# Kernel optimization log

Hardware: AMD Instinct MI355X
Metric: run time of the kernel (lower is better)

Reference implementation:

```python
import jax, jax.numpy as jnp
import numpy as np

DIM = 1024
H = 16
HD = 64

def setup_inputs() -> dict:
    key = jax.random.key(0)
    ks = jax.random.split(key, 5)
    x = jax.random.normal(ks[0], (2, 2048, DIM), dtype=jnp.float32)
    gamma = jnp.ones((DIM,), jnp.float32)
    beta = jnp.zeros((DIM,), jnp.float32)
    w_qkv = jax.random.normal(ks[1], (DIM, 3 * H * HD), dtype=jnp.float32) * (DIM ** -0.5)
    w_out = jax.random.normal(ks[2], (H * HD, DIM), dtype=jnp.float32) * ((H * HD) ** -0.5)
    b_out = jnp.zeros((DIM,), jnp.float32)
    return {"x": x, "gamma": gamma, "beta": beta, "w_qkv": w_qkv, "w_out": w_out, "b_out": b_out}

def reference(x, gamma, beta, w_qkv, w_out, b_out):
    # LayerNorm (pre-norm)
    mu = jnp.mean(x, axis=-1, keepdims=True)
    var = jnp.var(x, axis=-1, keepdims=True)
    xn = (x - mu) * jax.lax.rsqrt(var + 1e-5) * gamma + beta
    # QKV projection (no bias)
    qkv = xn @ w_qkv  # (b, n, 3*h*hd)
    q, k, v = jnp.split(qkv, 3, axis=-1)
    b, n, _ = x.shape
    split = lambda t: t.reshape(b, n, H, HD).transpose(0, 2, 1, 3)  # b h n d
    q, k, v = split(q), split(k), split(v)
    scale = HD ** -0.5
    scores = jnp.einsum('bhqd,bhkd->bhqk', q, k) * scale
    weights = jax.nn.softmax(scores, axis=-1)
    attn = jnp.einsum('bhqk,bhkd->bhqd', weights, v)  # b h n d
    attn = attn.transpose(0, 2, 1, 3).reshape(b, n, H * HD)
    # output projection (dropout is identity in eval)
    return attn @ w_out + b_out
```

## Files before the change

### kernel.cpp

```cpp
#include <hip/hip_runtime.h>
#include <hip/hip_bf16.h>


typedef _Float16 f16x8 __attribute__((ext_vector_type(8)));
typedef _Float16 f16x4 __attribute__((ext_vector_type(4)));
typedef float    f32x4 __attribute__((ext_vector_type(4)));

#define DIM   1024
#define NH    16
#define HD2   64
#define SEQ   2048
#define ROWS  4096
#define QKVN  3072

__device__ __forceinline__ void async_copy16(void* lds, const void* gsrc) {
    __builtin_amdgcn_global_load_lds(
        (const __attribute__((address_space(1))) unsigned int*)gsrc,
        (__attribute__((address_space(3))) unsigned int*)lds, 16, 0, 0);
}

__global__ __launch_bounds__(256) void prologue_kernel(
    const float* __restrict__ x, const float* __restrict__ gamma,
    const float* __restrict__ beta, _Float16* __restrict__ xn,
    const float* __restrict__ w_qkv, _Float16* __restrict__ wqkvT,
    const float* __restrict__ w_out, _Float16* __restrict__ woutT) {
    __shared__ float smem[32 * 33];
    const int bid = blockIdx.x;
    const int t = threadIdx.x;
    if (bid < ROWS) {
        const int row = bid;
        const float4 v = reinterpret_cast<const float4*>(x + (size_t)row * DIM)[t];
        float s1 = v.x + v.y + v.z + v.w;
        float s2 = v.x * v.x + v.y * v.y + v.z * v.z + v.w * v.w;
        for (int off = 32; off; off >>= 1) {
            s1 += __shfl_down(s1, off);
            s2 += __shfl_down(s2, off);
        }
        const int wv = t >> 6, lane = t & 63;
        if (lane == 0) { smem[wv * 2] = s1; smem[wv * 2 + 1] = s2; }
        __syncthreads();
        s1 = smem[0] + smem[2] + smem[4] + smem[6];
        s2 = smem[1] + smem[3] + smem[5] + smem[7];
        const float mu = s1 * (1.0f / DIM);
        const float var = s2 * (1.0f / DIM) - mu * mu;
        const float rstd = rsqrtf(var + 1e-5f);
        const float4 g = reinterpret_cast<const float4*>(gamma)[t];
        const float4 bb = reinterpret_cast<const float4*>(beta)[t];
        f16x4 o;
        o[0] = (_Float16)((v.x - mu) * rstd * g.x + bb.x);
        o[1] = (_Float16)((v.y - mu) * rstd * g.y + bb.y);
        o[2] = (_Float16)((v.z - mu) * rstd * g.z + bb.z);
        o[3] = (_Float16)((v.w - mu) * rstd * g.w + bb.w);
        reinterpret_cast<f16x4*>(xn + (size_t)row * DIM)[t] = o;
        return;
    }
    const float* in;
    _Float16* out;
    int C, bx, by;
    if (bid < ROWS + (QKVN / 32) * (DIM / 32)) {
        const int q = bid - ROWS;
        in = w_qkv; out = wqkvT; C = QKVN;
        bx = q % (QKVN / 32); by = q / (QKVN / 32);
    } else {
        const int q = bid - ROWS - (QKVN / 32) * (DIM / 32);
        in = w_out; out = woutT; C = DIM;
        bx = q % (DIM / 32); by = q / (DIM / 32);
    }
    const int R = DIM;
    const int c0 = bx * 32, r0 = by * 32;
    const int tx = t & 31, ty = t >> 5;
    float (*tile)[33] = reinterpret_cast<float(*)[33]>(smem);
#pragma unroll
    for (int i = 0; i < 4; i++)
        tile[ty + i * 8][tx] = in[(size_t)(r0 + ty + i * 8) * C + c0 + tx];
    __syncthreads();
#pragma unroll
    for (int i = 0; i < 4; i++)
        out[(size_t)(c0 + ty + i * 8) * R + r0 + tx] = (_Float16)tile[tx][ty + i * 8];
}

__global__ __launch_bounds__(256) void gemm_qkv_kernel(
    const _Float16* __restrict__ A, const _Float16* __restrict__ Bt,
    _Float16* __restrict__ qk, _Float16* __restrict__ vT, int K) {
    __shared__ _Float16 Al[2][128 * 32];
    __shared__ _Float16 Bl[2][128 * 32];
    const int t = threadIdx.x, wv = t >> 6, lane = t & 63;
    const int lg = lane >> 4, lr = lane & 15;
    const int wr = wv >> 1, wc = wv & 1;
    const int m0 = blockIdx.y * 128, n0 = blockIdx.x * 128;

    f32x4 acc[4][4] = {};

    const int srow = t >> 2, sk = (t & 3) * 8;
    const _Float16* Ag0 = A + (size_t)(m0 + srow) * K + sk;
    const _Float16* Bg0 = Bt + (size_t)(n0 + srow) * K + sk;

    auto STAGE = [&](int buf, int k0) {
        _Float16* Alw = &Al[buf][wv * 512];
        _Float16* Blw = &Bl[buf][wv * 512];
        async_copy16(Alw,        Ag0 + k0);
        async_copy16(Alw + 2048, Ag0 + (size_t)64 * K + k0);
        async_copy16(Blw,        Bg0 + k0);
        async_copy16(Blw + 2048, Bg0 + (size_t)64 * K + k0);
    };

    STAGE(0, 0);
    asm volatile("s_waitcnt vmcnt(0)" ::: "memory");
    __builtin_amdgcn_s_barrier();
    int cur = 0;
    for (int k0 = 0; k0 < K; k0 += 32) {
        if (k0 + 32 < K) STAGE(cur ^ 1, k0 + 32);
        const _Float16* Ab = &Al[cur][0];
        const _Float16* Bb = &Bl[cur][0];
        f16x8 af[4], bfr[4];
#pragma unroll
        for (int m = 0; m < 4; m++)
            af[m] = *reinterpret_cast<const f16x8*>(&Ab[(wr * 64 + m * 16 + lr) * 32 + lg * 8]);
#pragma unroll
        for (int n = 0; n < 4; n++)
            bfr[n] = *reinterpret_cast<const f16x8*>(&Bb[(wc * 64 + n * 16 + lr) * 32 + lg * 8]);
#pragma unroll
        for (int m = 0; m < 4; m++)
#pragma unroll
            for (int n = 0; n < 4; n++)
                acc[m][n] = __builtin_amdgcn_mfma_f32_16x16x32_f16(af[m], bfr[n], acc[m][n], 0, 0, 0);
        asm volatile("s_waitcnt vmcnt(0)" ::: "memory");
        __builtin_amdgcn_s_barrier();
        cur ^= 1;
    }

    if (n0 < 2 * DIM) {
#pragma unroll
        for (int m = 0; m < 4; m++) {
            const int row = m0 + wr * 64 + m * 16 + lg * 4;
#pragma unroll
            for (int n = 0; n < 4; n++) {
                const int col = n0 + wc * 64 + n * 16 + lr;
#pragma unroll
                for (int jj = 0; jj < 4; jj++)
                    qk[(size_t)(row + jj) * 2048 + col] = (_Float16)acc[m][n][jj];
            }
        }
    } else {
#pragma unroll
        for (int m = 0; m < 4; m++) {
            const int row = m0 + wr * 64 + m * 16 + lg * 4;
            const int b = row >> 11, nn = row & 2047;
#pragma unroll
            for (int n = 0; n < 4; n++) {
                const int vcol = n0 + wc * 64 + n * 16 + lr - 2 * DIM;
                f16x4 pk;
#pragma unroll
                for (int jj = 0; jj < 4; jj++) pk[jj] = (_Float16)acc[m][n][jj];
                *reinterpret_cast<f16x4*>(&vT[(size_t)(b * 1024 + vcol) * SEQ + nn]) = pk;
            }
        }
    }
}

__global__ __launch_bounds__(256) void gemm_out_kernel(
    const _Float16* __restrict__ A, const _Float16* __restrict__ Bt,
    float* __restrict__ C, const float* __restrict__ bias, int N, int K) {
    __shared__ _Float16 Al[2][128 * 32];
    __shared__ _Float16 Bl[2][64 * 32];
    const int t = threadIdx.x, wv = t >> 6, lane = t & 63;
    const int lg = lane >> 4, lr = lane & 15;
    const int wr = wv >> 1, wc = wv & 1;
    const int m0 = blockIdx.y * 128, n0 = blockIdx.x * 64;

    f32x4 acc[4][2] = {};

    const int srow = t >> 2, sk = (t & 3) * 8;
    const _Float16* Ag0 = A + (size_t)(m0 + srow) * K + sk;
    const _Float16* Bg0 = Bt + (size_t)(n0 + srow) * K + sk;

    auto STAGE = [&](int buf, int k0) {
        _Float16* Alw = &Al[buf][wv * 512];
        _Float16* Blw = &Bl[buf][wv * 512];
        async_copy16(Alw,        Ag0 + k0);
        async_copy16(Alw + 2048, Ag0 + (size_t)64 * K + k0);
        async_copy16(Blw,        Bg0 + k0);
    };

    STAGE(0, 0);
    asm volatile("s_waitcnt vmcnt(0)" ::: "memory");
    __builtin_amdgcn_s_barrier();
    int cur = 0;
    for (int k0 = 0; k0 < K; k0 += 32) {
        if (k0 + 32 < K) STAGE(cur ^ 1, k0 + 32);
        const _Float16* Ab = &Al[cur][0];
        const _Float16* Bb = &Bl[cur][0];
        f16x8 af[4], bfr[2];
#pragma unroll
        for (int m = 0; m < 4; m++)
            af[m] = *reinterpret_cast<const f16x8*>(&Ab[(wr * 64 + m * 16 + lr) * 32 + lg * 8]);
#pragma unroll
        for (int n = 0; n < 2; n++)
            bfr[n] = *reinterpret_cast<const f16x8*>(&Bb[(wc * 32 + n * 16 + lr) * 32 + lg * 8]);
#pragma unroll
        for (int m = 0; m < 4; m++)
#pragma unroll
            for (int n = 0; n < 2; n++)
                acc[m][n] = __builtin_amdgcn_mfma_f32_16x16x32_f16(af[m], bfr[n], acc[m][n], 0, 0, 0);
        asm volatile("s_waitcnt vmcnt(0)" ::: "memory");
        __builtin_amdgcn_s_barrier();
        cur ^= 1;
    }

#pragma unroll
    for (int m = 0; m < 4; m++) {
        const int row = m0 + wr * 64 + m * 16 + lg * 4;
#pragma unroll
        for (int n = 0; n < 2; n++) {
            const int col = n0 + wc * 32 + n * 16 + lr;
            const float bo = bias[col];
#pragma unroll
            for (int jj = 0; jj < 4; jj++)
                C[(size_t)(row + jj) * N + col] = acc[m][n][jj] + bo;
        }
    }
}

__global__ __launch_bounds__(256, 2) void attn_fa_kernel(
    const _Float16* __restrict__ qk, const _Float16* __restrict__ vT,
    _Float16* __restrict__ attn) {
    const int id = blockIdx.x;
    const int nid = (id & 7) * 64 + (id >> 3);
    const int bh = nid >> 4, b = bh >> 4, h = bh & 15;
    const int q0 = (nid & 15) * 128;
    const int t = threadIdx.x, wv = t >> 6, lane = t & 63;
    const int lg = lane >> 4, lr = lane & 15;

    __shared__ _Float16 Kl[2][64][72];
    __shared__ _Float16 Vt[2][64][72];

    const _Float16* qb = qk + (size_t)(b * SEQ + q0 + wv * 32 + lr) * 2048 + h * HD2;
    f16x8 qf[2][2];
    qf[0][0] = *reinterpret_cast<const f16x8*>(qb + lg * 8);
    qf[0][1] = *reinterpret_cast<const f16x8*>(qb + 32 + lg * 8);
    qf[1][0] = *reinterpret_cast<const f16x8*>(qb + (size_t)16 * 2048 + lg * 8);
    qf[1][1] = *reinterpret_cast<const f16x8*>(qb + (size_t)16 * 2048 + 32 + lg * 8);
#pragma unroll
    for (int qs = 0; qs < 2; qs++) {
        qf[qs][0] = qf[qs][0] * (_Float16)0.125f;
        qf[qs][1] = qf[qs][1] * (_Float16)0.125f;
    }

    f32x4 o[2][4] = {};
    float mrun[2] = {-INFINITY, -INFINITY}, lrun[2] = {0.f, 0.f};

    const int sr = t >> 3, sc = (t & 7) * 8;
    const _Float16* kbase = qk + (size_t)(b * SEQ + sr) * 2048 + DIM + h * HD2 + sc;
    const _Float16* vbase = vT + (size_t)(bh * HD2 + sr) * SEQ + sc;

    f16x8 rk0 = *reinterpret_cast<const f16x8*>(kbase);
    f16x8 rk1 = *reinterpret_cast<const f16x8*>(kbase + (size_t)32 * 2048);
    f16x8 rv0 = *reinterpret_cast<const f16x8*>(vbase);
    f16x8 rv1 = *reinterpret_cast<const f16x8*>(vbase + (size_t)32 * SEQ);
    *reinterpret_cast<f16x8*>(&Kl[0][sr][sc])      = rk0;
    *reinterpret_cast<f16x8*>(&Kl[0][sr + 32][sc]) = rk1;
    *reinterpret_cast<f16x8*>(&Vt[0][sr][sc])      = rv0;
    *reinterpret_cast<f16x8*>(&Vt[0][sr + 32][sc]) = rv1;
    rk0 = *reinterpret_cast<const f16x8*>(kbase + (size_t)64 * 2048);
    rk1 = *reinterpret_cast<const f16x8*>(kbase + (size_t)96 * 2048);
    rv0 = *reinterpret_cast<const f16x8*>(vbase + 64);
    rv1 = *reinterpret_cast<const f16x8*>(vbase + (size_t)32 * SEQ + 64);
    asm volatile("s_waitcnt lgkmcnt(0)" ::: "memory");
    __builtin_amdgcn_s_barrier();

    int p = 0;
    for (int kv0 = 0; kv0 < SEQ; kv0 += 64, p ^= 1) {
        if (kv0 + 64 < SEQ) {
            *reinterpret_cast<f16x8*>(&Kl[p ^ 1][sr][sc])      = rk0;
            *reinterpret_cast<f16x8*>(&Kl[p ^ 1][sr + 32][sc]) = rk1;
            *reinterpret_cast<f16x8*>(&Vt[p ^ 1][sr][sc])      = rv0;
            *reinterpret_cast<f16x8*>(&Vt[p ^ 1][sr + 32][sc]) = rv1;
            if (kv0 + 128 < SEQ) {
                const _Float16* kp = kbase + (size_t)(kv0 + 128) * 2048;
                const _Float16* vp = vbase + (kv0 + 128);
                rk0 = *reinterpret_cast<const f16x8*>(kp);
                rk1 = *reinterpret_cast<const f16x8*>(kp + (size_t)32 * 2048);
                rv0 = *reinterpret_cast<const f16x8*>(vp);
                rv1 = *reinterpret_cast<const f16x8*>(vp + (size_t)32 * SEQ);
            }
        }

        f32x4 s[2][4];
#pragma unroll
        for (int n = 0; n < 4; n++) {
            f16x8 kf0 = *reinterpret_cast<const f16x8*>(&Kl[p][n * 16 + lr][lg * 8]);
            f16x8 kf1 = *reinterpret_cast<const f16x8*>(&Kl[p][n * 16 + lr][32 + lg * 8]);
            __builtin_amdgcn_s_setprio(1);
#pragma unroll
            for (int qs = 0; qs < 2; qs++) {
                f32x4 z = {0.f, 0.f, 0.f, 0.f};
                z = __builtin_amdgcn_mfma_f32_16x16x32_f16(kf0, qf[qs][0], z, 0, 0, 0);
                z = __builtin_amdgcn_mfma_f32_16x16x32_f16(kf1, qf[qs][1], z, 0, 0, 0);
                s[qs][n] = z;
            }
            __builtin_amdgcn_s_setprio(0);
        }

        f16x8 pa[2][2];
#pragma unroll
        for (int qs = 0; qs < 2; qs++) {
            float m1 = fmaxf(fmaxf(s[qs][0][0], s[qs][0][1]), fmaxf(s[qs][0][2], s[qs][0][3]));
#pragma unroll
            for (int n = 1; n < 4; n++)
                m1 = fmaxf(m1, fmaxf(fmaxf(s[qs][n][0], s[qs][n][1]), fmaxf(s[qs][n][2], s[qs][n][3])));
            m1 = fmaxf(m1, __shfl_xor(m1, 16));
            m1 = fmaxf(m1, __shfl_xor(m1, 32));
            if (!__all(m1 - mrun[qs] <= 8.f)) {
                const float mnew = fmaxf(mrun[qs], m1);
                const float corr = __expf(mrun[qs] - mnew);
                mrun[qs] = mnew;
                lrun[qs] *= corr;
#pragma unroll
                for (int dn = 0; dn < 4; dn++) o[qs][dn] *= corr;
            }
            float rsum = 0.f;
#pragma unroll
            for (int n = 0; n < 4; n++)
#pragma unroll
                for (int jj = 0; jj < 4; jj++) {
                    const float pv = __expf(s[qs][n][jj] - mrun[qs]);
                    s[qs][n][jj] = pv;
                    rsum += pv;
                }
            rsum += __shfl_xor(rsum, 16);
            rsum += __shfl_xor(rsum, 32);
            lrun[qs] += rsum;
#pragma unroll
            for (int m = 0; m < 2; m++) {
                f16x8 pv;
#pragma unroll
                for (int jj = 0; jj < 4; jj++) {
                    pv[jj]     = (_Float16)s[qs][2 * m][jj];
                    pv[4 + jj] = (_Float16)s[qs][2 * m + 1][jj];
                }
                pa[qs][m] = pv;
            }
        }

#pragma unroll
        for (int dn = 0; dn < 4; dn++) {
            const _Float16* vr = &Vt[p][dn * 16 + lr][0];
            f16x4 va0 = *reinterpret_cast<const f16x4*>(vr + lg * 4);
            f16x4 va1 = *reinterpret_cast<const f16x4*>(vr + 16 + lg * 4);
            f16x4 vb0 = *reinterpret_cast<const f16x4*>(vr + 32 + lg * 4);
            f16x4 vb1 = *reinterpret_cast<const f16x4*>(vr + 48 + lg * 4);
            f16x8 vf0, vf1;
#pragma unroll
            for (int j = 0; j < 4; j++) {
                vf0[j] = va0[j]; vf0[4 + j] = va1[j];
                vf1[j] = vb0[j]; vf1[4 + j] = vb1[j];
            }
            __builtin_amdgcn_s_setprio(1);
#pragma unroll
            for (int qs = 0; qs < 2; qs++) {
                o[qs][dn] = __builtin_amdgcn_mfma_f32_16x16x32_f16(vf0, pa[qs][0], o[qs][dn], 0, 0, 0);
                o[qs][dn] = __builtin_amdgcn_mfma_f32_16x16x32_f16(vf1, pa[qs][1], o[qs][dn], 0, 0, 0);
            }
            __builtin_amdgcn_s_setprio(0);
        }
        asm volatile("s_waitcnt lgkmcnt(0)" ::: "memory");
        __builtin_amdgcn_s_barrier();
    }

#pragma unroll
    for (int qs = 0; qs < 2; qs++) {
        const float inv = 1.0f / lrun[qs];
        const size_t orow = (size_t)(b * SEQ + q0 + wv * 32 + qs * 16 + lr);
#pragma unroll
        for (int dn = 0; dn < 4; dn++) {
            f16x4 pk;
#pragma unroll
            for (int jj = 0; jj < 4; jj++) pk[jj] = (_Float16)(o[qs][dn][jj] * inv);
            *reinterpret_cast<f16x4*>(&attn[orow * DIM + h * HD2 + dn * 16 + lg * 4]) = pk;
        }
    }
}

extern "C" void kernel_launch(void* const* d_in, const int* in_sizes, int n_in,
                              void* d_out, int out_size, void* d_ws, size_t ws_size,
                              hipStream_t stream) {
    const float* x     = (const float*)d_in[0];
    const float* gamma = (const float*)d_in[1];
    const float* beta  = (const float*)d_in[2];
    const float* w_qkv = (const float*)d_in[3];
    const float* w_out = (const float*)d_in[4];
    const float* b_out = (const float*)d_in[5];
    float* out = (float*)d_out;

    _Float16* ws    = (_Float16*)d_ws;
    _Float16* xn    = ws;
    _Float16* wqkvT = xn + (size_t)ROWS * DIM;
    _Float16* woutT = wqkvT + (size_t)QKVN * DIM;
    _Float16* qk    = woutT + (size_t)DIM * DIM;
    _Float16* vT    = qk + (size_t)ROWS * 2048;
    _Float16* attnb = xn;

    const int pro_blocks = ROWS + (QKVN / 32) * (DIM / 32) + (DIM / 32) * (DIM / 32);
    prologue_kernel<<<pro_blocks, 256, 0, stream>>>(x, gamma, beta, xn, w_qkv, wqkvT, w_out, woutT);
    gemm_qkv_kernel<<<dim3(QKVN / 128, ROWS / 128), 256, 0, stream>>>(xn, wqkvT, qk, vT, DIM);
    attn_fa_kernel<<<512, 256, 0, stream>>>(qk, vT, attnb);
    gemm_out_kernel<<<dim3(DIM / 64, ROWS / 128), 256, 0, stream>>>(attnb, woutT, out, b_out, DIM, DIM);
}
```

Before: 205.4 us.

## Halve attention query tile per block and remap GEMM blocks for XCD locality

The attention kernel now processes 64 query rows per block (16 per wave) instead of 128, doubling the grid to 1024 blocks and raising the occupancy hint to 4 blocks per CU. The LDS row pitch is padded from 72 to 76. Both GEMM kernels switch to a 1D grid with a swizzled block index so that consecutive blocks on each XCD share operand tiles. The aim is better CU utilization and L2 locality, at the cost of reloading each K/V tile twice as often per query.

New measurement: 208.9 us. About the same (+1.7%).

```diff
diff --git a/kernel.cpp b/kernel.cpp
--- a/kernel.cpp
+++ b/kernel.cpp
@@ -87,7 +87,10 @@
     const int t = threadIdx.x, wv = t >> 6, lane = t & 63;
     const int lg = lane >> 4, lr = lane & 15;
     const int wr = wv >> 1, wc = wv & 1;
-    const int m0 = blockIdx.y * 128, n0 = blockIdx.x * 128;
+    const int id = blockIdx.x;
+    const int nid = (id & 7) * 96 + (id >> 3);
+    const int bx = nid / 32, by = nid % 32;
+    const int m0 = by * 128, n0 = bx * 128;
 
     f32x4 acc[4][4] = {};
 
@@ -166,7 +169,10 @@
     const int t = threadIdx.x, wv = t >> 6, lane = t & 63;
     const int lg = lane >> 4, lr = lane & 15;
     const int wr = wv >> 1, wc = wv & 1;
-    const int m0 = blockIdx.y * 128, n0 = blockIdx.x * 64;
+    const int id = blockIdx.x;
+    const int nid = (id & 7) * 64 + (id >> 3);
+    const int bx = nid / 32, by = nid % 32;
+    const int m0 = by * 128, n0 = bx * 64;
 
     f32x4 acc[4][2] = {};
 
@@ -221,33 +227,27 @@
     }
 }
 
-__global__ __launch_bounds__(256, 2) void attn_fa_kernel(
+__global__ __launch_bounds__(256, 4) void attn_fa_kernel(
     const _Float16* __restrict__ qk, const _Float16* __restrict__ vT,
     _Float16* __restrict__ attn) {
     const int id = blockIdx.x;
-    const int nid = (id & 7) * 64 + (id >> 3);
-    const int bh = nid >> 4, b = bh >> 4, h = bh & 15;
-    const int q0 = (nid & 15) * 128;
+    const int nid = (id & 7) * 128 + (id >> 3);
+    const int bh = nid >> 5, b = bh >> 4, h = bh & 15;
+    const int q0 = (nid & 31) * 64;
     const int t = threadIdx.x, wv = t >> 6, lane = t & 63;
     const int lg = lane >> 4, lr = lane & 15;
 
-    __shared__ _Float16 Kl[2][64][72];
-    __shared__ _Float16 Vt[2][64][72];
-
-    const _Float16* qb = qk + (size_t)(b * SEQ + q0 + wv * 32 + lr) * 2048 + h * HD2;
-    f16x8 qf[2][2];
-    qf[0][0] = *reinterpret_cast<const f16x8*>(qb + lg * 8);
-    qf[0][1] = *reinterpret_cast<const f16x8*>(qb + 32 + lg * 8);
-    qf[1][0] = *reinterpret_cast<const f16x8*>(qb + (size_t)16 * 2048 + lg * 8);
-    qf[1][1] = *reinterpret_cast<const f16x8*>(qb + (size_t)16 * 2048 + 32 + lg * 8);
-#pragma unroll
-    for (int qs = 0; qs < 2; qs++) {
-        qf[qs][0] = qf[qs][0] * (_Float16)0.125f;
-        qf[qs][1] = qf[qs][1] * (_Float16)0.125f;
-    }
-
-    f32x4 o[2][4] = {};
-    float mrun[2] = {-INFINITY, -INFINITY}, lrun[2] = {0.f, 0.f};
+    __shared__ _Float16 Kl[2][64][76];
+    __shared__ _Float16 Vt[2][64][76];
+
+    const _Float16* qp = qk + (size_t)(b * SEQ + q0 + wv * 16 + lr) * 2048 + h * HD2;
+    f16x8 qf0 = *reinterpret_cast<const f16x8*>(qp + lg * 8);
+    f16x8 qf1 = *reinterpret_cast<const f16x8*>(qp + 32 + lg * 8);
+    qf0 = qf0 * (_Float16)0.125f;
+    qf1 = qf1 * (_Float16)0.125f;
+
+    f32x4 o[4] = {};
+    float mrun = -INFINITY, lrun = 0.f;
 
     const int sr = t >> 3, sc = (t & 7) * 8;
     const _Float16* kbase = qk + (size_t)(b * SEQ + sr) * 2048 + DIM + h * HD2 + sc;
@@ -285,61 +285,56 @@
             }
         }
 
-        f32x4 s[2][4];
+        f32x4 s[4];
 #pragma unroll
         for (int n = 0; n < 4; n++) {
             f16x8 kf0 = *reinterpret_cast<const f16x8*>(&Kl[p][n * 16 + lr][lg * 8]);
             f16x8 kf1 = *reinterpret_cast<const f16x8*>(&Kl[p][n * 16 + lr][32 + lg * 8]);
+            f32x4 z = {0.f, 0.f, 0.f, 0.f};
             __builtin_amdgcn_s_setprio(1);
-#pragma unroll
-            for (int qs = 0; qs < 2; qs++) {
-                f32x4 z = {0.f, 0.f, 0.f, 0.f};
-                z = __builtin_amdgcn_mfma_f32_16x16x32_f16(kf0, qf[qs][0], z, 0, 0, 0);
-                z = __builtin_amdgcn_mfma_f32_16x16x32_f16(kf1, qf[qs][1], z, 0, 0, 0);
-                s[qs][n] = z;
-            }
+            z = __builtin_amdgcn_mfma_f32_16x16x32_f16(kf0, qf0, z, 0, 0, 0);
+            z = __builtin_amdgcn_mfma_f32_16x16x32_f16(kf1, qf1, z, 0, 0, 0);
             __builtin_amdgcn_s_setprio(0);
-        }
-
-        f16x8 pa[2][2];
-#pragma unroll
-        for (int qs = 0; qs < 2; qs++) {
-            float m1 = fmaxf(fmaxf(s[qs][0][0], s[qs][0][1]), fmaxf(s[qs][0][2], s[qs][0][3]));
-#pragma unroll
-            for (int n = 1; n < 4; n++)
-                m1 = fmaxf(m1, fmaxf(fmaxf(s[qs][n][0], s[qs][n][1]), fmaxf(s[qs][n][2], s[qs][n][3])));
-            m1 = fmaxf(m1, __shfl_xor(m1, 16));
-            m1 = fmaxf(m1, __shfl_xor(m1, 32));
-            if (!__all(m1 - mrun[qs] <= 8.f)) {
-                const float mnew = fmaxf(mrun[qs], m1);
-                const float corr = __expf(mrun[qs] - mnew);
-                mrun[qs] = mnew;
-                lrun[qs] *= corr;
-#pragma unroll
-                for (int dn = 0; dn < 4; dn++) o[qs][dn] *= corr;
-            }
-            float rsum = 0.f;
-#pragma unroll
-            for (int n = 0; n < 4; n++)
-#pragma unroll
-                for (int jj = 0; jj < 4; jj++) {
-                    const float pv = __expf(s[qs][n][jj] - mrun[qs]);
-                    s[qs][n][jj] = pv;
-                    rsum += pv;
-                }
-            rsum += __shfl_xor(rsum, 16);
-            rsum += __shfl_xor(rsum, 32);
-            lrun[qs] += rsum;
-#pragma unroll
-            for (int m = 0; m < 2; m++) {
-                f16x8 pv;
-#pragma unroll
-                for (int jj = 0; jj < 4; jj++) {
-                    pv[jj]     = (_Float16)s[qs][2 * m][jj];
-                    pv[4 + jj] = (_Float16)s[qs][2 * m + 1][jj];
-                }
-                pa[qs][m] = pv;
-            }
+            s[n] = z;
+        }
+
+        float m1 = fmaxf(fmaxf(s[0][0], s[0][1]), fmaxf(s[0][2], s[0][3]));
+#pragma unroll
+        for (int n = 1; n < 4; n++)
+            m1 = fmaxf(m1, fmaxf(fmaxf(s[n][0], s[n][1]), fmaxf(s[n][2], s[n][3])));
+        m1 = fmaxf(m1, __shfl_xor(m1, 16));
+        m1 = fmaxf(m1, __shfl_xor(m1, 32));
+        if (!__all(m1 - mrun <= 8.f)) {
+            const float mnew = fmaxf(mrun, m1);
+            const float corr = __expf(mrun - mnew);
+            mrun = mnew;
+            lrun *= corr;
+#pragma unroll
+            for (int dn = 0; dn < 4; dn++) o[dn] *= corr;
+        }
+        float rsum = 0.f;
+#pragma unroll
+        for (int n = 0; n < 4; n++)
+#pragma unroll
+            for (int jj = 0; jj < 4; jj++) {
+                const float pv = __expf(s[n][jj] - mrun);
+                s[n][jj] = pv;
+                rsum += pv;
+            }
+        rsum += __shfl_xor(rsum, 16);
+        rsum += __shfl_xor(rsum, 32);
+        lrun += rsum;
+
+        f16x8 pa[2];
+#pragma unroll
+        for (int m = 0; m < 2; m++) {
+            f16x8 pv;
+#pragma unroll
+            for (int jj = 0; jj < 4; jj++) {
+                pv[jj]     = (_Float16)s[2 * m][jj];
+                pv[4 + jj] = (_Float16)s[2 * m + 1][jj];
+            }
+            pa[m] = pv;
         }
 
 #pragma unroll
@@ -356,28 +351,22 @@
                 vf1[j] = vb0[j]; vf1[4 + j] = vb1[j];
             }
             __builtin_amdgcn_s_setprio(1);
-#pragma unroll
-            for (int qs = 0; qs < 2; qs++) {
-                o[qs][dn] = __builtin_amdgcn_mfma_f32_16x16x32_f16(vf0, pa[qs][0], o[qs][dn], 0, 0, 0);
-                o[qs][dn] = __builtin_amdgcn_mfma_f32_16x16x32_f16(vf1, pa[qs][1], o[qs][dn], 0, 0, 0);
-            }
+            o[dn] = __builtin_amdgcn_mfma_f32_16x16x32_f16(vf0, pa[0], o[dn], 0, 0, 0);
+            o[dn] = __builtin_amdgcn_mfma_f32_16x16x32_f16(vf1, pa[1], o[dn], 0, 0, 0);
             __builtin_amdgcn_s_setprio(0);
         }
         asm volatile("s_waitcnt lgkmcnt(0)" ::: "memory");
         __builtin_amdgcn_s_barrier();
     }
 
-#pragma unroll
-    for (int qs = 0; qs < 2; qs++) {
-        const float inv = 1.0f / lrun[qs];
-        const size_t orow = (size_t)(b * SEQ + q0 + wv * 32 + qs * 16 + lr);
-#pragma unroll
-        for (int dn = 0; dn < 4; dn++) {
-            f16x4 pk;
-#pragma unroll
-            for (int jj = 0; jj < 4; jj++) pk[jj] = (_Float16)(o[qs][dn][jj] * inv);
-            *reinterpret_cast<f16x4*>(&attn[orow * DIM + h * HD2 + dn * 16 + lg * 4]) = pk;
-        }
+    const float inv = 1.0f / lrun;
+    const size_t orow = (size_t)(b * SEQ + q0 + wv * 16 + lr);
+#pragma unroll
+    for (int dn = 0; dn < 4; dn++) {
+        f16x4 pk;
+#pragma unroll
+        for (int jj = 0; jj < 4; jj++) pk[jj] = (_Float16)(o[dn][jj] * inv);
+        *reinterpret_cast<f16x4*>(&attn[orow * DIM + h * HD2 + dn * 16 + lg * 4]) = pk;
     }
 }
 
@@ -402,7 +391,7 @@
 
     const int pro_blocks = ROWS + (QKVN / 32) * (DIM / 32) + (DIM / 32) * (DIM / 32);
     prologue_kernel<<<pro_blocks, 256, 0, stream>>>(x, gamma, beta, xn, w_qkv, wqkvT, w_out, woutT);
-    gemm_qkv_kernel<<<dim3(QKVN / 128, ROWS / 128), 256, 0, stream>>>(xn, wqkvT, qk, vT, DIM);
-    attn_fa_kernel<<<512, 256, 0, stream>>>(qk, vT, attnb);
-    gemm_out_kernel<<<dim3(DIM / 64, ROWS / 128), 256, 0, stream>>>(attnb, woutT, out, b_out, DIM, DIM);
-}
+    gemm_qkv_kernel<<<768, 256, 0, stream>>>(xn, wqkvT, qk, vT, DIM);
+    attn_fa_kernel<<<1024, 256, 0, stream>>>(qk, vT, attnb);
+    gemm_out_kernel<<<512, 256, 0, stream>>>(attnb, woutT, out, b_out, DIM, DIM);
+}
```
